# Performance work log

Measured on AMD Instinct MI355X. Metric: run time of the kernel, lower is better.

Reference implementation:

```python
import jax, jax.numpy as jnp
import numpy as np

NUM_CLASSES = 100000
FEAT_DIM = 128
BATCH = 16384
LOSS_WEIGHT = 0.01


def setup_inputs() -> dict:
    key = jax.random.key(0)
    k1, k2, k3 = jax.random.split(key, 3)
    y = jax.random.randint(k1, (BATCH,), 0, NUM_CLASSES, dtype=jnp.int64)
    feat = jax.random.normal(k2, (BATCH, FEAT_DIM), dtype=jnp.float32)
    centers = jax.random.normal(k3, (NUM_CLASSES, FEAT_DIM), dtype=jnp.float32)
    return {"y": y, "feat": feat, "centers": centers}


def reference(y, feat, centers):
    # hist: per-class counts (torch.histc with unit-width bins over [0, num_classes])
    counts = jax.ops.segment_sum(jnp.ones((feat.shape[0],), feat.dtype), y,
                                 num_segments=NUM_CLASSES)  # [C]
    # per-class mean of features; zeros for empty classes (sum is 0 there)
    feat_sum = jax.ops.segment_sum(feat, y, num_segments=NUM_CLASSES)  # [C, D]
    feat_mean = feat_sum / jnp.maximum(counts, 1.0)[:, None]
    ratio = counts / (1.0 + counts)  # hist / (1 + hist)
    centers_grad = ratio[:, None] * (centers - feat_mean)  # [C, D]
    diff = feat - centers[y]  # gather centers per sample
    loss = LOSS_WEIGHT * 0.5 * jnp.sum(diff * diff)
    return (loss, centers_grad)
```

## Files before the change

kernel.cpp:

```cpp
#include <hip/hip_runtime.h>


#define BATCH   16384
#define FEAT    128
#define NCLASS  100000
#define LOSS_W  0.01f
#define CAP     32
#define NGRAD   12500
#define K1_BLK  1024

typedef float v4f __attribute__((ext_vector_type(4)));

__global__ __launch_bounds__(256)
void k_hist_loss(const int* __restrict__ y,
                 const float* __restrict__ feat,
                 const float* __restrict__ centers,
                 int* __restrict__ cnt,
                 int* __restrict__ bucket,
                 float* __restrict__ partial) {
    int tid = blockIdx.x * 256 + threadIdx.x;

    if (tid < BATCH) {
        int c = y[tid];
        int r = atomicAdd(cnt + c, 1);
        if (r < CAP) bucket[c * CAP + r] = tid;
    }

    int hw = tid >> 5;
    int q  = tid & 31;
    float ls = 0.0f;
    #pragma unroll
    for (int s = 0; s < 2; s++) {
        int i = hw * 2 + s;
        int c = y[i];
        v4f f  = *((const v4f*)(feat    + (size_t)i * FEAT) + q);
        v4f ce = *((const v4f*)(centers + (size_t)c * FEAT) + q);
        v4f d = f - ce;
        ls += d.x*d.x + d.y*d.y + d.z*d.z + d.w*d.w;
    }

    #pragma unroll
    for (int off = 32; off > 0; off >>= 1)
        ls += __shfl_down(ls, off, 64);
    __shared__ float smem[4];
    if ((threadIdx.x & 63) == 0) smem[threadIdx.x >> 6] = ls;
    __syncthreads();
    if (threadIdx.x == 0)
        partial[blockIdx.x] = smem[0] + smem[1] + smem[2] + smem[3];
}

__global__ __launch_bounds__(256)
void k_grad(const float* __restrict__ centers,
            const int* __restrict__ cnt,
            const int* __restrict__ bucket,
            const float* __restrict__ feat,
            float* __restrict__ grad,
            const float* __restrict__ partial,
            float* __restrict__ loss) {
    if (blockIdx.x == NGRAD) {
        v4f v = ((const v4f*)partial)[threadIdx.x];
        float s = v.x + v.y + v.z + v.w;
        #pragma unroll
        for (int off = 32; off > 0; off >>= 1)
            s += __shfl_down(s, off, 64);
        __shared__ float sm[4];
        if ((threadIdx.x & 63) == 0) sm[threadIdx.x >> 6] = s;
        __syncthreads();
        if (threadIdx.x == 0)
            *loss = LOSS_W * 0.5f * (sm[0] + sm[1] + sm[2] + sm[3]);
        return;
    }

    int wid  = (blockIdx.x * 256 + threadIdx.x) >> 6;
    int lane = threadIdx.x & 63;
    int c    = wid * 2 + (lane >> 5);
    int q    = lane & 31;
    int n = cnt[c];

    v4f ce = (v4f)(0.0f);
    if (n > 0)
        ce = __builtin_nontemporal_load(
                 (const v4f*)(centers + (size_t)c * FEAT) + q);

    int m = n < CAP ? n : CAP;
    v4f acc = (v4f)(0.0f);
    for (int k = 0; k < m; k++) {
        int i = bucket[c * CAP + k];
        v4f f = __builtin_nontemporal_load(
                    (const v4f*)(feat + (size_t)i * FEAT) + q);
        acc += f;
    }

    v4f o = (v4f)(0.0f);
    if (n > 0) {
        float inv   = 1.0f / (float)n;
        float ratio = (float)n / (1.0f + (float)n);
        o = ratio * (ce - acc * inv);
    }
    __builtin_nontemporal_store(o, (v4f*)(grad + (size_t)c * FEAT) + q);
}

extern "C" void kernel_launch(void* const* d_in, const int* in_sizes, int n_in,
                              void* d_out, int out_size, void* d_ws, size_t ws_size,
                              hipStream_t stream) {
    const int*   y       = (const int*)d_in[0];
    const float* feat    = (const float*)d_in[1];
    const float* centers = (const float*)d_in[2];

    float* loss = (float*)d_out;
    float* grad = (float*)d_out + 1;

    int*   cnt     = (int*)d_ws;
    int*   bucket  = cnt + NCLASS;
    float* partial = (float*)(bucket + (size_t)NCLASS * CAP);

    (void)hipMemsetAsync(cnt, 0, (size_t)NCLASS * sizeof(int), stream);

    k_hist_loss<<<K1_BLK, 256, 0, stream>>>(y, feat, centers, cnt, bucket, partial);

    k_grad<<<NGRAD + 1, 256, 0, stream>>>(
        centers, cnt, bucket, feat, grad, partial, loss);
}
```

Baseline: 117.6 us.

## Fuse memset, histogram/loss, and gradient into one cooperative persistent kernel

Replaces the memset plus two kernel launches with a single cooperative kernel of 1024 blocks that zeroes the counts, computes loss partials, builds the class buckets, and then loops persistently over gradient tiles, using grid-wide syncs between phases. This removes launch overhead and the separate memset. In exchange it adds two grid barriers, leaves only 16 threads per block doing the atomics, and lowers gradient-phase parallelism to a grid-stride loop over 1024 blocks.

New measurement: 290.3 us. 147% more time.

```diff
diff --git a/kernel.cpp b/kernel.cpp
--- a/kernel.cpp
+++ b/kernel.cpp
@@ -1,4 +1,7 @@
 #include <hip/hip_runtime.h>
+#include <hip/hip_cooperative_groups.h>
+
+namespace cg = cooperative_groups;
 
 
 #define BATCH   16384
@@ -7,24 +10,23 @@
 #define LOSS_W  0.01f
 #define CAP     32
 #define NGRAD   12500
-#define K1_BLK  1024
+#define GRID    1024
 
 typedef float v4f __attribute__((ext_vector_type(4)));
 
-__global__ __launch_bounds__(256)
-void k_hist_loss(const int* __restrict__ y,
-                 const float* __restrict__ feat,
-                 const float* __restrict__ centers,
-                 int* __restrict__ cnt,
-                 int* __restrict__ bucket,
-                 float* __restrict__ partial) {
+__global__ __launch_bounds__(256, 4)
+void k_fused(const int* __restrict__ y,
+             const float* __restrict__ feat,
+             const float* __restrict__ centers,
+             int* __restrict__ cnt,
+             int* __restrict__ bucket,
+             float* __restrict__ partial,
+             float* __restrict__ grad,
+             float* __restrict__ loss) {
+    cg::grid_group gg = cg::this_grid();
     int tid = blockIdx.x * 256 + threadIdx.x;
 
-    if (tid < BATCH) {
-        int c = y[tid];
-        int r = atomicAdd(cnt + c, 1);
-        if (r < CAP) bucket[c * CAP + r] = tid;
-    }
+    if (tid < NCLASS) cnt[tid] = 0;
 
     int hw = tid >> 5;
     int q  = tid & 31;
@@ -38,7 +40,6 @@
         v4f d = f - ce;
         ls += d.x*d.x + d.y*d.y + d.z*d.z + d.w*d.w;
     }
-
     #pragma unroll
     for (int off = 32; off > 0; off >>= 1)
         ls += __shfl_down(ls, off, 64);
@@ -47,17 +48,19 @@
     __syncthreads();
     if (threadIdx.x == 0)
         partial[blockIdx.x] = smem[0] + smem[1] + smem[2] + smem[3];
-}
 
-__global__ __launch_bounds__(256)
-void k_grad(const float* __restrict__ centers,
-            const int* __restrict__ cnt,
-            const int* __restrict__ bucket,
-            const float* __restrict__ feat,
-            float* __restrict__ grad,
-            const float* __restrict__ partial,
-            float* __restrict__ loss) {
-    if (blockIdx.x == NGRAD) {
+    gg.sync();
+
+    if (threadIdx.x < 16) {
+        int s = blockIdx.x * 16 + threadIdx.x;
+        int c = y[s];
+        int r = atomicAdd(cnt + c, 1);
+        if (r < CAP) bucket[c * CAP + r] = s;
+    }
+
+    gg.sync();
+
+    if (blockIdx.x == 0) {
         v4f v = ((const v4f*)partial)[threadIdx.x];
         float s = v.x + v.y + v.z + v.w;
         #pragma unroll
@@ -68,36 +71,38 @@
         __syncthreads();
         if (threadIdx.x == 0)
             *loss = LOSS_W * 0.5f * (sm[0] + sm[1] + sm[2] + sm[3]);
-        return;
     }
 
-    int wid  = (blockIdx.x * 256 + threadIdx.x) >> 6;
     int lane = threadIdx.x & 63;
-    int c    = wid * 2 + (lane >> 5);
-    int q    = lane & 31;
-    int n = cnt[c];
+    int wq   = threadIdx.x >> 6;
+    int p    = lane & 31;
+    for (int u = blockIdx.x; u < NGRAD; u += GRID) {
+        int wid = u * 4 + wq;
+        int c   = wid * 2 + (lane >> 5);
+        int n = cnt[c];
 
-    v4f ce = (v4f)(0.0f);
-    if (n > 0)
-        ce = __builtin_nontemporal_load(
-                 (const v4f*)(centers + (size_t)c * FEAT) + q);
+        v4f ce = (v4f)(0.0f);
+        if (n > 0)
+            ce = __builtin_nontemporal_load(
+                     (const v4f*)(centers + (size_t)c * FEAT) + p);
 
-    int m = n < CAP ? n : CAP;
-    v4f acc = (v4f)(0.0f);
-    for (int k = 0; k < m; k++) {
-        int i = bucket[c * CAP + k];
-        v4f f = __builtin_nontemporal_load(
-                    (const v4f*)(feat + (size_t)i * FEAT) + q);
-        acc += f;
+        int m = n < CAP ? n : CAP;
+        v4f acc = (v4f)(0.0f);
+        for (int k = 0; k < m; k++) {
+            int i = bucket[c * CAP + k];
+            v4f f = __builtin_nontemporal_load(
+                        (const v4f*)(feat + (size_t)i * FEAT) + p);
+            acc += f;
+        }
+
+        v4f o = (v4f)(0.0f);
+        if (n > 0) {
+            float inv   = 1.0f / (float)n;
+            float ratio = (float)n / (1.0f + (float)n);
+            o = ratio * (ce - acc * inv);
+        }
+        __builtin_nontemporal_store(o, (v4f*)(grad + (size_t)c * FEAT) + p);
     }
-
-    v4f o = (v4f)(0.0f);
-    if (n > 0) {
-        float inv   = 1.0f / (float)n;
-        float ratio = (float)n / (1.0f + (float)n);
-        o = ratio * (ce - acc * inv);
-    }
-    __builtin_nontemporal_store(o, (v4f*)(grad + (size_t)c * FEAT) + q);
 }
 
 extern "C" void kernel_launch(void* const* d_in, const int* in_sizes, int n_in,
@@ -114,10 +119,10 @@
     int*   bucket  = cnt + NCLASS;
     float* partial = (float*)(bucket + (size_t)NCLASS * CAP);
 
-    (void)hipMemsetAsync(cnt, 0, (size_t)NCLASS * sizeof(int), stream);
-
-    k_hist_loss<<<K1_BLK, 256, 0, stream>>>(y, feat, centers, cnt, bucket, partial);
-
-    k_grad<<<NGRAD + 1, 256, 0, stream>>>(
-        centers, cnt, bucket, feat, grad, partial, loss);
+    void* args[] = {(void*)&y, (void*)&feat, (void*)&centers,
+                    (void*)&cnt, (void*)&bucket, (void*)&partial,
+                    (void*)&grad, (void*)&loss};
+    (void)hipLaunchCooperativeKernel((const void*)k_fused,
+                                     dim3(GRID), dim3(256),
+                                     args, 0, stream);
 }
```
